# Kernel optimization log

Measured on AMD Instinct MI355X. Metric: run time of the kernel, lower is better.

The kernel has to match this reference:

```python
import jax, jax.numpy as jnp
import numpy as np

WIDTHS = [2, 3, 5, 8, 13, 21, 34, 55, 89, 26]  # ragged one-hot feature widths, sum = 256
NSEG = len(WIDTHS)
B, IN = 8192, 256
LAYOUT = [1024, 1024, 1024, 256]
EPS = 1e-5  # BatchNorm1d default eps
TAU = 1.0


def setup_inputs() -> dict:
    key = jax.random.key(0)
    ks = iter(jax.random.split(key, 64))
    inp = {"x": jax.random.normal(next(ks), (B, IN), jnp.float32)}
    prev = IN
    for i, fc in enumerate(LAYOUT):
        inp[f"W{i}"] = jax.random.normal(next(ks), (fc, prev), jnp.float32) / np.float32(np.sqrt(prev))
        inp[f"b{i}"] = 0.01 * jax.random.normal(next(ks), (fc,), jnp.float32)
        if i + 1 < len(LAYOUT):  # Residual blocks carry BatchNorm params (eval mode)
            inp[f"g{i}"] = 1.0 + 0.1 * jax.random.normal(next(ks), (fc,), jnp.float32)
            inp[f"be{i}"] = 0.1 * jax.random.normal(next(ks), (fc,), jnp.float32)
            inp[f"rm{i}"] = 0.1 * jax.random.normal(next(ks), (fc,), jnp.float32)
            inp[f"rv{i}"] = 0.75 + 0.5 * jax.random.uniform(next(ks), (fc,), dtype=jnp.float32)
        prev += fc
    inp["seg_ids"] = jnp.asarray(np.repeat(np.arange(NSEG), WIDTHS), jnp.int32)  # [256]
    return inp


def _residual(x, W, b, g, be, rm, rv):
    # Linear -> eval-mode BatchNorm1d -> ReLU -> concat([out, input])
    h = x @ W.T + b
    h = (h - rm) * (g * jax.lax.rsqrt(rv + EPS)) + be
    return jnp.concatenate([jax.nn.relu(h), x], axis=1)


def _segment_softmax(x, seg_ids):
    # Fused segmented softmax over ragged feature groups (replaces per-feature Python loop)
    xt = x.T / TAU                                            # [F, B]
    m = jax.ops.segment_max(xt, seg_ids, num_segments=NSEG)   # [NSEG, B]
    e = jnp.exp(xt - m[seg_ids])
    s = jax.ops.segment_sum(e, seg_ids, num_segments=NSEG)
    return (e / s[seg_ids]).T                                 # [B, F]


def reference(x, W0, b0, g0, be0, rm0, rv0, W1, b1, g1, be1, rm1, rv1,
              W2, b2, g2, be2, rm2, rv2, W3, b3, seg_ids):
    h = _residual(x, W0, b0, g0, be0, rm0, rv0)   # [B, 1280]
    h = _residual(h, W1, b1, g1, be1, rm1, rv1)   # [B, 2304]
    h = _residual(h, W2, b2, g2, be2, rm2, rv2)   # [B, 3328]
    h = h @ W3.T + b3                              # [B, 256]
    return _segment_softmax(h, seg_ids)
```

## Files before the change

### kernel.cpp

```cpp
#include <hip/hip_runtime.h>
#include <hip/hip_fp16.h>


#define LDH 3328
#define NROWS 8192

typedef _Float16 f16x8 __attribute__((ext_vector_type(8)));
typedef _Float16 f16x4 __attribute__((ext_vector_type(4)));
typedef float f32x4 __attribute__((ext_vector_type(4)));

__constant__ int c_bnd[11] = {0, 2, 5, 10, 18, 31, 52, 86, 141, 230, 256};

__device__ __forceinline__ void async_cp16(const _Float16* g, _Float16* l) {
  __builtin_amdgcn_global_load_lds(
      (__attribute__((address_space(1))) void*)g,
      (__attribute__((address_space(3))) void*)l, 16, 0, 0);
}

__device__ __forceinline__ _Float16 f2h(float f) { return (_Float16)f; }

__global__ void cvt_kernel(const float* __restrict__ src,
                           _Float16* __restrict__ dst, int n4) {
  int i = blockIdx.x * blockDim.x + threadIdx.x;
  if (i >= n4) return;
  const float4 v = *(const float4*)&src[(size_t)i * 4];
  f16x4 h = {f2h(v.x), f2h(v.y), f2h(v.z), f2h(v.w)};
  *(f16x4*)&dst[(size_t)i * 4] = h;
}

__global__ void stagex_kernel(const float* __restrict__ x,
                              _Float16* __restrict__ H) {
  int i = blockIdx.x * blockDim.x + threadIdx.x;
  int row = i >> 6;
  int c = (i & 63) * 4;
  const float4 v = *(const float4*)&x[(size_t)row * 256 + c];
  f16x4 h = {f2h(v.x), f2h(v.y), f2h(v.z), f2h(v.w)};
  *(f16x4*)&H[(size_t)row * LDH + 3072 + c] = h;
}

template <int FUSE>
__launch_bounds__(256, 2) __global__
void gemm_kernel(const _Float16* __restrict__ A, int ldA, int K,
                 const _Float16* __restrict__ W,
                 const float* __restrict__ bias, const float* __restrict__ g,
                 const float* __restrict__ be, const float* __restrict__ rm,
                 const float* __restrict__ rv,
                 _Float16* __restrict__ outH, int outOff,
                 float* __restrict__ outF, int ldF) {
  __shared__ _Float16 Alds[128 * 64];
  __shared__ _Float16 Blds[128 * 64];

  const int tid = threadIdx.x;
  const int lane = tid & 63;
  const int wave = tid >> 6;
  const int wr = wave >> 1;
  const int wc = wave & 1;
  const int row0 = blockIdx.x * 128;
  const int col0 = blockIdx.y * 128;
  const int lr = lane >> 3;
  const int ls = lane & 7;
  const int lc = ls ^ lr;
  const int fr = lane & 15;
  const int q = lane >> 4;

  f32x4 acc[4][4] = {};

  for (int k0 = 0; k0 < K; k0 += 64) {
    __syncthreads();
#pragma unroll
    for (int it = 0; it < 4; ++it) {
      const int rl = it * 32 + wave * 8;
      const _Float16* ga =
          A + (size_t)(row0 + rl + lr) * ldA + k0 + lc * 8;
      async_cp16(ga, &Alds[rl * 64]);
      const _Float16* gb =
          W + (size_t)(col0 + rl + lr) * K + k0 + lc * 8;
      async_cp16(gb, &Blds[rl * 64]);
    }
    __syncthreads();

#pragma unroll
    for (int kq = 0; kq < 2; ++kq) {
      f16x8 av[4], bv[4];
#pragma unroll
      for (int t = 0; t < 4; ++t) {
        const int ra = wr * 64 + t * 16 + fr;
        av[t] = *(const f16x8*)&Alds[ra * 64 + (((q + 4 * kq) ^ (ra & 7)) * 8)];
        const int rb = wc * 64 + t * 16 + fr;
        bv[t] = *(const f16x8*)&Blds[rb * 64 + (((q + 4 * kq) ^ (rb & 7)) * 8)];
      }
#pragma unroll
      for (int tm = 0; tm < 4; ++tm)
#pragma unroll
        for (int tn = 0; tn < 4; ++tn)
          acc[tm][tn] = __builtin_amdgcn_mfma_f32_16x16x32_f16(
              av[tm], bv[tn], acc[tm][tn], 0, 0, 0);
    }
  }

#pragma unroll
  for (int tn = 0; tn < 4; ++tn) {
    const int n = col0 + wc * 64 + tn * 16 + fr;
    if constexpr (FUSE == 1) {
      const float alpha = g[n] * rsqrtf(rv[n] + 1e-5f);
      const float beta = (bias[n] - rm[n]) * alpha + be[n];
#pragma unroll
      for (int tm = 0; tm < 4; ++tm) {
        const int rbase = row0 + wr * 64 + tm * 16 + q * 4;
#pragma unroll
        for (int r = 0; r < 4; ++r) {
          float v = acc[tm][tn][r] * alpha + beta;
          v = fmaxf(v, 0.0f);
          outH[(size_t)(rbase + r) * LDH + outOff + n] = f2h(v);
        }
      }
    } else {
      const float bb = bias[n];
#pragma unroll
      for (int tm = 0; tm < 4; ++tm) {
        const int rbase = row0 + wr * 64 + tm * 16 + q * 4;
#pragma unroll
        for (int r = 0; r < 4; ++r)
          outF[(size_t)(rbase + r) * ldF + n] = acc[tm][tn][r] + bb;
      }
    }
  }
}

__global__ void segsoftmax_kernel(float* __restrict__ out,
                                  const int* __restrict__ segids) {
  __shared__ float vals[256];
  __shared__ float red[10];
  const int row = blockIdx.x;
  const int l = threadIdx.x;
  float4 v = *(float4*)&out[(size_t)row * 256 + l * 4];
  *(float4*)&vals[l * 4] = v;
  __syncthreads();
  if (l < 10) {
    float m = -1e30f;
    for (int j = c_bnd[l]; j < c_bnd[l + 1]; ++j) m = fmaxf(m, vals[j]);
    red[l] = m;
  }
  __syncthreads();
  const int4 s4 = *(const int4*)&segids[l * 4];
  float4 e;
  e.x = expf(v.x - red[s4.x]);
  e.y = expf(v.y - red[s4.y]);
  e.z = expf(v.z - red[s4.z]);
  e.w = expf(v.w - red[s4.w]);
  *(float4*)&vals[l * 4] = e;
  __syncthreads();
  if (l < 10) {
    float s = 0.0f;
    for (int j = c_bnd[l]; j < c_bnd[l + 1]; ++j) s += vals[j];
    red[l] = s;
  }
  __syncthreads();
  float4 o;
  o.x = e.x / red[s4.x];
  o.y = e.y / red[s4.y];
  o.z = e.z / red[s4.z];
  o.w = e.w / red[s4.w];
  *(float4*)&out[(size_t)row * 256 + l * 4] = o;
}

extern "C" void kernel_launch(void* const* d_in, const int* in_sizes, int n_in,
                              void* d_out, int out_size, void* d_ws,
                              size_t ws_size, hipStream_t stream) {
  const float* x = (const float*)d_in[0];
  const float* W0 = (const float*)d_in[1];
  const float* b0 = (const float*)d_in[2];
  const float* g0 = (const float*)d_in[3];
  const float* be0 = (const float*)d_in[4];
  const float* rm0 = (const float*)d_in[5];
  const float* rv0 = (const float*)d_in[6];
  const float* W1 = (const float*)d_in[7];
  const float* b1 = (const float*)d_in[8];
  const float* g1 = (const float*)d_in[9];
  const float* be1 = (const float*)d_in[10];
  const float* rm1 = (const float*)d_in[11];
  const float* rv1 = (const float*)d_in[12];
  const float* W2 = (const float*)d_in[13];
  const float* b2 = (const float*)d_in[14];
  const float* g2 = (const float*)d_in[15];
  const float* be2 = (const float*)d_in[16];
  const float* rm2 = (const float*)d_in[17];
  const float* rv2 = (const float*)d_in[18];
  const float* W3 = (const float*)d_in[19];
  const float* b3 = (const float*)d_in[20];
  const int* seg = (const int*)d_in[21];
  float* out = (float*)d_out;

  _Float16* H = (_Float16*)d_ws;
  size_t off = (size_t)NROWS * LDH;
  _Float16* Wh0 = H + off; off += 1024 * 256;
  _Float16* Wh1 = H + off; off += 1024 * 1280;
  _Float16* Wh2 = H + off; off += 1024 * 2304;
  _Float16* Wh3 = H + off;

  cvt_kernel<<<256, 256, 0, stream>>>(W0, Wh0, 65536);
  cvt_kernel<<<1280, 256, 0, stream>>>(W1, Wh1, 327680);
  cvt_kernel<<<2304, 256, 0, stream>>>(W2, Wh2, 589824);
  cvt_kernel<<<832, 256, 0, stream>>>(W3, Wh3, 212992);
  stagex_kernel<<<2048, 256, 0, stream>>>(x, H);

  dim3 blk(256);
  gemm_kernel<1><<<dim3(64, 8), blk, 0, stream>>>(
      H + 3072, LDH, 256, Wh0, b0, g0, be0, rm0, rv0, H, 2048, nullptr, 0);
  gemm_kernel<1><<<dim3(64, 8), blk, 0, stream>>>(
      H + 2048, LDH, 1280, Wh1, b1, g1, be1, rm1, rv1, H, 1024, nullptr, 0);
  gemm_kernel<1><<<dim3(64, 8), blk, 0, stream>>>(
      H + 1024, LDH, 2304, Wh2, b2, g2, be2, rm2, rv2, H, 0, nullptr, 0);
  gemm_kernel<0><<<dim3(64, 2), blk, 0, stream>>>(
      H, LDH, 3328, Wh3, b3, nullptr, nullptr, nullptr, nullptr, nullptr, 0,
      out, 256);
  segsoftmax_kernel<<<8192, 64, 0, stream>>>(out, seg);
}
```

Before: 272.9 us.

## Split-K final GEMM with atomic accumulation and merge weight conversions

The final 256-column GEMM previously launched only 128 blocks. It now splits K=3328 into four 832-wide slices, giving 512 blocks, and accumulates partial results with float atomicAdd into an output buffer that a new kernel pre-initializes with the bias. The four weight conversion launches are merged into one kernel, and the launch bounds hint is raised to 4 blocks per SM. The atomics add contention and make the summation order nondeterministic, and the extra init kernel writes the output once more.

```diff
diff --git a/kernel.cpp b/kernel.cpp
--- a/kernel.cpp
+++ b/kernel.cpp
@@ -19,13 +19,32 @@
 
 __device__ __forceinline__ _Float16 f2h(float f) { return (_Float16)f; }
 
-__global__ void cvt_kernel(const float* __restrict__ src,
-                           _Float16* __restrict__ dst, int n4) {
+__global__ void cvt_all_kernel(const float* __restrict__ s0,
+                               const float* __restrict__ s1,
+                               const float* __restrict__ s2,
+                               const float* __restrict__ s3,
+                               _Float16* __restrict__ d0,
+                               _Float16* __restrict__ d1,
+                               _Float16* __restrict__ d2,
+                               _Float16* __restrict__ d3,
+                               int n0, int n1, int n2, int n3) {
   int i = blockIdx.x * blockDim.x + threadIdx.x;
-  if (i >= n4) return;
-  const float4 v = *(const float4*)&src[(size_t)i * 4];
+  const float* s;
+  _Float16* d;
+  if (i < n0) {
+    s = s0; d = d0;
+  } else if (i < n1) {
+    s = s1 - (size_t)n0 * 4; d = d1 - (size_t)n0 * 4;
+  } else if (i < n2) {
+    s = s2 - (size_t)n1 * 4; d = d2 - (size_t)n1 * 4;
+  } else if (i < n3) {
+    s = s3 - (size_t)n2 * 4; d = d3 - (size_t)n2 * 4;
+  } else {
+    return;
+  }
+  const float4 v = *(const float4*)&s[(size_t)i * 4];
   f16x4 h = {f2h(v.x), f2h(v.y), f2h(v.z), f2h(v.w)};
-  *(f16x4*)&dst[(size_t)i * 4] = h;
+  *(f16x4*)&d[(size_t)i * 4] = h;
 }
 
 __global__ void stagex_kernel(const float* __restrict__ x,
@@ -38,15 +57,24 @@
   *(f16x4*)&H[(size_t)row * LDH + 3072 + c] = h;
 }
 
+__global__ void init_out_kernel(float* __restrict__ out,
+                                const float* __restrict__ bias) {
+  int i = blockIdx.x * blockDim.x + threadIdx.x;
+  int c = (i & 63) * 4;
+  const float4 b = *(const float4*)&bias[c];
+  *(float4*)&out[(size_t)i * 4] = b;
+}
+
 template <int FUSE>
-__launch_bounds__(256, 2) __global__
+__launch_bounds__(256, 4) __global__
 void gemm_kernel(const _Float16* __restrict__ A, int ldA, int K,
+                 int kBeg, int kEnd,
                  const _Float16* __restrict__ W,
                  const float* __restrict__ bias, const float* __restrict__ g,
                  const float* __restrict__ be, const float* __restrict__ rm,
                  const float* __restrict__ rv,
                  _Float16* __restrict__ outH, int outOff,
-                 float* __restrict__ outF, int ldF) {
+                 float* __restrict__ outF, int ldF, int nColBlk) {
   __shared__ _Float16 Alds[128 * 64];
   __shared__ _Float16 Blds[128 * 64];
 
@@ -56,7 +84,11 @@
   const int wr = wave >> 1;
   const int wc = wave & 1;
   const int row0 = blockIdx.x * 128;
-  const int col0 = blockIdx.y * 128;
+  const int cb = blockIdx.y % nColBlk;
+  const int ks = blockIdx.y / nColBlk;
+  const int col0 = cb * 128;
+  const int k0b = kBeg + ks * (kEnd - kBeg);
+  const int k0e = k0b + (kEnd - kBeg);
   const int lr = lane >> 3;
   const int ls = lane & 7;
   const int lc = ls ^ lr;
@@ -65,7 +97,7 @@
 
   f32x4 acc[4][4] = {};
 
-  for (int k0 = 0; k0 < K; k0 += 64) {
+  for (int k0 = k0b; k0 < k0e; k0 += 64) {
     __syncthreads();
 #pragma unroll
     for (int it = 0; it < 4; ++it) {
@@ -115,13 +147,12 @@
         }
       }
     } else {
-      const float bb = bias[n];
 #pragma unroll
       for (int tm = 0; tm < 4; ++tm) {
         const int rbase = row0 + wr * 64 + tm * 16 + q * 4;
 #pragma unroll
         for (int r = 0; r < 4; ++r)
-          outF[(size_t)(rbase + r) * ldF + n] = acc[tm][tn][r] + bb;
+          atomicAdd(&outF[(size_t)(rbase + r) * ldF + n], acc[tm][tn][r]);
       }
     }
   }
@@ -198,21 +229,24 @@
   _Float16* Wh2 = H + off; off += 1024 * 2304;
   _Float16* Wh3 = H + off;
 
-  cvt_kernel<<<256, 256, 0, stream>>>(W0, Wh0, 65536);
-  cvt_kernel<<<1280, 256, 0, stream>>>(W1, Wh1, 327680);
-  cvt_kernel<<<2304, 256, 0, stream>>>(W2, Wh2, 589824);
-  cvt_kernel<<<832, 256, 0, stream>>>(W3, Wh3, 212992);
+  const int n0 = 65536, n1 = n0 + 327680, n2 = n1 + 589824, n3 = n2 + 212992;
+  cvt_all_kernel<<<(n3 + 255) / 256, 256, 0, stream>>>(
+      W0, W1, W2, W3, Wh0, Wh1, Wh2, Wh3, n0, n1, n2, n3);
   stagex_kernel<<<2048, 256, 0, stream>>>(x, H);
+  init_out_kernel<<<2048, 256, 0, stream>>>(out, b3);
 
   dim3 blk(256);
   gemm_kernel<1><<<dim3(64, 8), blk, 0, stream>>>(
-      H + 3072, LDH, 256, Wh0, b0, g0, be0, rm0, rv0, H, 2048, nullptr, 0);
+      H + 3072, LDH, 256, 0, 256, Wh0, b0, g0, be0, rm0, rv0, H, 2048,
+      nullptr, 0, 8);
   gemm_kernel<1><<<dim3(64, 8), blk, 0, stream>>>(
-      H + 2048, LDH, 1280, Wh1, b1, g1, be1, rm1, rv1, H, 1024, nullptr, 0);
+      H + 2048, LDH, 1280, 0, 1280, Wh1, b1, g1, be1, rm1, rv1, H, 1024,
+      nullptr, 0, 8);
   gemm_kernel<1><<<dim3(64, 8), blk, 0, stream>>>(
-      H + 1024, LDH, 2304, Wh2, b2, g2, be2, rm2, rv2, H, 0, nullptr, 0);
-  gemm_kernel<0><<<dim3(64, 2), blk, 0, stream>>>(
-      H, LDH, 3328, Wh3, b3, nullptr, nullptr, nullptr, nullptr, nullptr, 0,
-      out, 256);
+      H + 1024, LDH, 2304, 0, 2304, Wh2, b2, g2, be2, rm2, rv2, H, 0,
+      nullptr, 0, 8);
+  gemm_kernel<0><<<dim3(64, 8), blk, 0, stream>>>(
+      H, LDH, 3328, 0, 832, Wh3, nullptr, nullptr, nullptr, nullptr, nullptr,
+      nullptr, 0, out, 256, 2);
   segsoftmax_kernel<<<8192, 64, 0, stream>>>(out, seg);
 }
```

After: 254.3 us. 1.07x faster.
